# Kernel optimization log

Hardware: AMD Instinct MI355X
Metric: run time of the kernel (lower is better)

The kernel has to match this reference:

```python
import jax, jax.numpy as jnp
import numpy as np

B, S, D, H, KD, HID = 8, 1024, 512, 8, 64, 32


def setup_inputs() -> dict:
    key = jax.random.key(0)
    ks = jax.random.split(key, 13)
    s = 0.05
    return {
        "src": jax.random.normal(ks[0], (B, S, D), jnp.float32),
        "Wq": jax.random.normal(ks[1], (H, KD, D), jnp.float32) * s,
        "Wk": jax.random.normal(ks[2], (H, KD, D), jnp.float32) * s,
        "Wv": jax.random.normal(ks[3], (H, KD, D), jnp.float32) * s,
        "c_raw": jnp.ones((H,), jnp.float32),              # nn.Parameter(1.0) per head
        "L": jnp.full((H,), 2.0, jnp.float32),             # nn.Parameter(2.0) per head
        "w1": jax.random.normal(ks[4], (H, HID), jnp.float32) * s,   # Linear(1,HID) weight
        "b1": jax.random.normal(ks[5], (H, HID), jnp.float32) * s,
        "W2": jax.random.normal(ks[6], (H, HID, HID), jnp.float32) * s,  # [out,in]
        "b2": jax.random.normal(ks[7], (H, HID), jnp.float32) * s,
        "w3": jax.random.normal(ks[8], (H, HID), jnp.float32) * s,   # Linear(HID,1) weight
        "b3": jax.random.normal(ks[9], (H,), jnp.float32) * s,
        "Wo": jax.random.normal(ks[10], (D, D), jnp.float32) * s,
    }


def _gelu(x):
    return jax.nn.gelu(x, approximate=False)  # torch nn.GELU default (erf)


def reference(src, Wq, Wk, Wv, c_raw, L, w1, b1, W2, b2, w3, b3, Wo):
    Bc, Sc, Dc = src.shape
    Hh, Kd = Wq.shape[0], Wq.shape[1]
    # ---- FIRE bias: raw[i,j] = log1p(c*(i-j)) / log1p(c*max(L, i+1)) for j<i else 0
    ii = jnp.arange(Sc, dtype=jnp.float32)[:, None]   # [S,1]
    jj = jnp.arange(Sc, dtype=jnp.float32)[None, :]   # [1,S]
    d = ii - jj                                       # [S,S]
    c = jax.nn.softplus(c_raw)[:, None, None]         # [H,1,1]
    num = jnp.log1p(c * jnp.where(d > 0, d, 1.0)[None])          # safe for d<=0
    den = jnp.log1p(c * jnp.maximum(L[:, None, None], ii[None] + 1.0))
    raw = jnp.where(d[None] > 0, num / den, 0.0)      # [H,S,S]
    # ---- f_theta MLP applied elementwise (Linear(1,h)->GELU->Linear(h,h)->GELU->Linear(h,1))
    h1 = _gelu(raw[..., None] * w1[:, None, None, :] + b1[:, None, None, :])   # [H,S,S,HID]
    h2 = _gelu(jnp.einsum('hijk,hlk->hijl', h1, W2) + b2[:, None, None, :])    # [H,S,S,HID]
    bias = jnp.einsum('hijk,hk->hij', h2, w3) + b3[:, None, None]              # [H,S,S]
    # ---- causal mask (strict upper triangle -> -inf)
    causal = jnp.arange(Sc)[None, :] > jnp.arange(Sc)[:, None]
    bias = jnp.where(causal[None], -jnp.inf, bias)
    # ---- attention per head
    q = jnp.einsum('bsd,hkd->bhsk', src, Wq)
    k = jnp.einsum('bsd,hkd->bhsk', src, Wk)
    v = jnp.einsum('bsd,hkd->bhsk', src, Wv)
    logits = jnp.einsum('bhik,bhjk->bhij', q, k) / jnp.sqrt(jnp.float32(Kd)) + bias[None]
    attn = jax.nn.softmax(logits, axis=-1)
    o = jnp.einsum('bhij,bhjk->bhik', attn, v)        # [B,H,S,KD]
    o = jnp.transpose(o, (0, 2, 1, 3)).reshape(Bc, Sc, Hh * Kd)  # concat heads
    return o @ Wo.T
```

## Files before the change

kernel.cpp:

```cpp
#include <hip/hip_runtime.h>
#include <math.h>

#define S_LEN 1024
#define NHEAD 8
#define BATCH 8
#define KDIM  64
#define HID   32
#define NT    2048
#define TRI(q) ((q) * ((q) + 1) / 2)

typedef __attribute__((ext_vector_type(8))) short bf16x8;
typedef __attribute__((ext_vector_type(4))) float f32x4;
typedef unsigned short ushort_t;

__device__ inline ushort_t f2bf(float f) {
  union { float f; unsigned u; } v; v.f = f;
  unsigned u = v.u;
  return (ushort_t)((u + 0x7FFFu + ((u >> 16) & 1u)) >> 16);
}
__device__ inline float bf2f(ushort_t u) {
  union { unsigned x; float f; } v; v.x = ((unsigned)u) << 16; return v.f;
}

__device__ inline void gl_lds16(const ushort_t* g, ushort_t* l) {
  __builtin_amdgcn_global_load_lds(
      (const __attribute__((address_space(1))) unsigned int*)g,
      (__attribute__((address_space(3))) unsigned int*)l, 16, 0, 0);
}

__global__ __launch_bounds__(256) void to_bf16(
    const float* __restrict__ s, const float* __restrict__ wq,
    const float* __restrict__ wk, const float* __restrict__ wv,
    const float* __restrict__ wo,
    ushort_t* __restrict__ sb, ushort_t* __restrict__ wqb,
    ushort_t* __restrict__ wkb, ushort_t* __restrict__ wvb,
    ushort_t* __restrict__ wob) {
  const int y = blockIdx.y;
  const float* src; ushort_t* dst; int n; float scale = 1.0f;
  if (y == 0)      { src = s;  dst = sb;  n = 4194304; }
  else if (y == 1) { src = wq; dst = wqb; n = 262144; scale = 0.125f; }
  else if (y == 2) { src = wk; dst = wkb; n = 262144; }
  else if (y == 3) { src = wv; dst = wvb; n = 262144; }
  else             { src = wo; dst = wob; n = 262144; }
  const int i = (blockIdx.x * 256 + threadIdx.x) * 4;
  if (i < n) {
    float4 v = *(const float4*)&src[i];
    ushort4 o;
    o.x = f2bf(v.x * scale); o.y = f2bf(v.y * scale);
    o.z = f2bf(v.z * scale); o.w = f2bf(v.w * scale);
    *(ushort4*)&dst[i] = o;
  }
}

__global__ __launch_bounds__(256) void fire_tables(
    const float* __restrict__ c_raw, const float* __restrict__ Lp,
    const float* __restrict__ w1, const float* __restrict__ b1,
    const float* __restrict__ W2, const float* __restrict__ b2,
    const float* __restrict__ w3, const float* __restrict__ b3,
    float* __restrict__ num_g, float* __restrict__ rden_g,
    float* __restrict__ gtab_g) {
  __shared__ float h1s[8][33];
  const int h = blockIdx.y;
  const int tid = threadIdx.x;
  const int pl = tid >> 5;
  const int j = tid & 31;
  const int pt = blockIdx.x * 8 + pl;
  const float cr = c_raw[h];
  const float c = (cr > 20.f) ? cr : log1pf(expf(cr));
  const int gid = blockIdx.x * 256 + tid;
  if (gid < S_LEN) {
    num_g[h * S_LEN + gid] = log1pf(c * (float)gid);
    rden_g[h * S_LEN + gid] = 1.0f / log1pf(c * fmaxf(Lp[h], (float)(gid + 1)));
  }
  const float x = (float)pt * (1.0f / NT);
  float v = x * w1[h * HID + j] + b1[h * HID + j];
  h1s[pl][j] = 0.5f * v * (1.0f + erff(v * 0.70710678118f));
  __syncthreads();
  float s = b2[h * HID + j];
  const float* w2r = W2 + ((size_t)(h * HID + j)) * HID;
  #pragma unroll
  for (int k = 0; k < HID; ++k) s += w2r[k] * h1s[pl][k];
  float g = 0.5f * s * (1.0f + erff(s * 0.70710678118f));
  float y = w3[h * HID + j] * g;
  #pragma unroll
  for (int off = 1; off < 32; off <<= 1) y += __shfl_xor(y, off);
  if (j == 0 && pt <= NT) gtab_g[h * (NT + 1) + pt] = y + b3[h];
}

__global__ __launch_bounds__(256) void fire_bias_pre(
    const float* __restrict__ num_g, const float* __restrict__ rden_g,
    const float* __restrict__ gtab_g, ushort_t* __restrict__ biaspre) {
  __shared__ float gtab_s[NT + 1];
  __shared__ float num_s[S_LEN];
  __shared__ float rden_s[64];
  const int tid = threadIdx.x;
  const int h = blockIdx.y;
  const int tileIdx = blockIdx.x;
  int qt = 0;
  while (TRI(qt + 1) <= tileIdx) ++qt;
  const int t = tileIdx - TRI(qt);
  for (int i = tid; i <= NT; i += 256) gtab_s[i] = gtab_g[h * (NT + 1) + i];
  for (int i = tid; i < S_LEN; i += 256) num_s[i] = num_g[h * S_LEN + i];
  if (tid < 64) rden_s[tid] = rden_g[h * S_LEN + qt * 64 + tid];
  __syncthreads();
  const int lane = tid & 63, w = tid >> 6, quad = lane >> 4, l16 = lane & 15;
  ushort_t vals[16];
  #pragma unroll
  for (int nb = 0; nb < 4; ++nb) {
    #pragma unroll
    for (int r = 0; r < 4; ++r) {
      const int iloc = w * 16 + quad * 4 + r;
      const int i = qt * 64 + iloc;
      const int j = t * 64 + nb * 16 + l16;
      ushort_t out;
      if (j > i) {
        out = 0xFF80;
      } else {
        const int d = i - j;
        float x = num_s[d] * rden_s[iloc];
        float tf = x * (float)NT;
        int it = (int)tf; it = it < (NT - 1) ? it : (NT - 1);
        float fr = tf - (float)it;
        float ga = gtab_s[it];
        out = f2bf(ga + (gtab_s[it + 1] - ga) * fr);
      }
      vals[nb * 4 + r] = out;
    }
  }
  ushort_t* dst = &biaspre[(((size_t)h * 136 + tileIdx) * 256 + tid) * 16];
  uint4 lo, hi;
  #pragma unroll
  for (int v = 0; v < 8; ++v) { ((ushort_t*)&lo)[v] = vals[v]; ((ushort_t*)&hi)[v] = vals[v + 8]; }
  *(uint4*)dst = lo;
  *(uint4*)(dst + 8) = hi;
}

__global__ __launch_bounds__(256) void gemm_bf16(
    const ushort_t* __restrict__ A,
    const ushort_t* __restrict__ W0, const ushort_t* __restrict__ W1,
    const ushort_t* __restrict__ W2w,
    void* __restrict__ out0, void* __restrict__ out1, void* __restrict__ out2,
    int scatter) {
  __shared__ __align__(16) ushort_t sAB[16384];
  ushort_t* sA = sAB;
  ushort_t* sB = sAB + 8192;
  const int tid = threadIdx.x;
  const int lane = tid & 63;
  const int w = tid >> 6;
  const int quad = lane >> 4;
  const int l16 = lane & 15;
  const int m0 = blockIdx.x * 128;
  const int n0 = blockIdx.y * 128;
  const int z = blockIdx.z;
  const ushort_t* Wp = (z == 0) ? W0 : (z == 1) ? W1 : W2w;
  void* outp = (z == 0) ? out0 : (z == 1) ? out1 : out2;
  const int mode = scatter ? ((z == 2) ? 2 : 1) : 0;

  f32x4 acc[2][8];
  #pragma unroll
  for (int s2 = 0; s2 < 2; ++s2)
    #pragma unroll
    for (int nb = 0; nb < 8; ++nb) acc[s2][nb] = (f32x4)0.0f;

  const int r8 = lane >> 3;
  const int gc = (lane & 7) ^ r8;
  const int sw = l16 & 7;

  for (int kt = 0; kt < 512; kt += 64) {
    __syncthreads();
    #pragma unroll
    for (int j = 0; j < 4; ++j) {
      const int row = j * 32 + w * 8 + r8;
      gl_lds16(&A[(size_t)(m0 + row) * 512 + kt + gc * 8], &sA[(j * 32 + w * 8) * 64]);
      gl_lds16(&Wp[(size_t)(n0 + row) * 512 + kt + gc * 8], &sB[(j * 32 + w * 8) * 64]);
    }
    __syncthreads();
    #pragma unroll
    for (int ks = 0; ks < 2; ++ks) {
      const int c = ks * 4 + quad;
      const int off = ((c ^ sw) * 8);
      bf16x8 a0 = *(bf16x8*)&sA[(w * 32 + l16) * 64 + off];
      bf16x8 a1 = *(bf16x8*)&sA[(w * 32 + 16 + l16) * 64 + off];
      #pragma unroll
      for (int nb = 0; nb < 8; ++nb) {
        bf16x8 bfr = *(bf16x8*)&sB[(nb * 16 + l16) * 64 + off];
        acc[0][nb] = __builtin_amdgcn_mfma_f32_16x16x32_bf16(a0, bfr, acc[0][nb], 0, 0, 0);
        acc[1][nb] = __builtin_amdgcn_mfma_f32_16x16x32_bf16(a1, bfr, acc[1][nb], 0, 0, 0);
      }
    }
  }

  if (mode == 2) {
    __syncthreads();
    #pragma unroll
    for (int s2 = 0; s2 < 2; ++s2)
      #pragma unroll
      for (int nb = 0; nb < 8; ++nb)
        #pragma unroll
        for (int r = 0; r < 4; ++r) {
          int nl = nb * 16 + l16;
          int ml = w * 32 + s2 * 16 + quad * 4 + r;
          sAB[nl * 128 + (((ml >> 3) ^ (nl & 7)) * 8) + (ml & 7)] = f2bf(acc[s2][nb][r]);
        }
    __syncthreads();
    const int nl = tid >> 1, halfm = tid & 1;
    const int ng = n0 + nl, hh = ng >> 6, kd = ng & 63;
    const int bb = m0 >> 10, sbase = m0 & 1023;
    ushort_t* vout = (ushort_t*)outp + (((size_t)(bb * NHEAD + hh)) * KDIM + kd) * S_LEN;
    #pragma unroll
    for (int c2 = 0; c2 < 8; ++c2) {
      int mc = halfm * 8 + c2;
      bf16x8 vr = *(bf16x8*)&sAB[nl * 128 + ((mc ^ (nl & 7)) * 8)];
      *(bf16x8*)&vout[sbase + mc * 8] = vr;
    }
    return;
  }
  #pragma unroll
  for (int s2 = 0; s2 < 2; ++s2) {
    #pragma unroll
    for (int nb = 0; nb < 8; ++nb) {
      #pragma unroll
      for (int r = 0; r < 4; ++r) {
        int m = m0 + w * 32 + s2 * 16 + quad * 4 + r;
        int n = n0 + nb * 16 + l16;
        float v = acc[s2][nb][r];
        if (mode == 1) {
          int bb = m >> 10, ss = m & 1023, hh = n >> 6, kd = n & 63;
          ((ushort_t*)outp)[(((size_t)(bb * NHEAD + hh)) * S_LEN + ss) * KDIM + kd] = f2bf(v);
        } else {
          ((float*)outp)[(size_t)m * 512 + n] = v;
        }
      }
    }
  }
}

__global__ __launch_bounds__(256) void fire_attn_mfma(
    const ushort_t* __restrict__ Qg, const ushort_t* __restrict__ Kg,
    const ushort_t* __restrict__ Vtg, const ushort_t* __restrict__ biaspre,
    ushort_t* __restrict__ Ob) {
  __shared__ __align__(16) ushort_t Ks[64][72];
  __shared__ __align__(16) ushort_t Vt[64][72];
  __shared__ __align__(16) ushort_t Ps[64][72];

  const int tid = threadIdx.x;
  const int lane = tid & 63;
  const int w = tid >> 6;
  const int quad = lane >> 4;
  const int l16 = lane & 15;
  const int g = blockIdx.x >> 6;
  const int qt = (g < 8) ? (15 - g) : (g - 8);
  const int bh = blockIdx.x & 63;
  const int h = bh & (NHEAD - 1);
  const int b = bh >> 3;

  const size_t qrow = (size_t)bh * S_LEN + qt * 64 + w * 16 + l16;
  bf16x8 aq0 = *(const bf16x8*)&Qg[qrow * KDIM + quad * 8];
  bf16x8 aq1 = *(const bf16x8*)&Qg[qrow * KDIM + 32 + quad * 8];

  const int krow = tid >> 2, kseg = tid & 3;
  const size_t kb = (size_t)bh * S_LEN * KDIM;
  const ushort_t* kptr = &Kg[kb + (size_t)krow * 64 + kseg * 16];
  const ushort_t* vptr = &Vtg[kb + (size_t)krow * 1024 + kseg * 16];
  const ushort_t* bptr = &biaspre[(((size_t)h * 136 + TRI(qt)) * 256 + tid) * 16];

  uint4 kr0 = *(const uint4*)(kptr);
  uint4 kr1 = *(const uint4*)(kptr + 8);
  uint4 vr0 = *(const uint4*)(vptr);
  uint4 vr1 = *(const uint4*)(vptr + 8);

  f32x4 o[4];
  float ll[4];
  #pragma unroll
  for (int nb = 0; nb < 4; ++nb) o[nb] = (f32x4)0.0f;
  #pragma unroll
  for (int r = 0; r < 4; ++r) ll[r] = 0.f;
  const int i0loc = w * 16 + quad * 4;

  for (int t = 0; t <= qt; ++t) {
    __syncthreads();
    *(uint4*)&Ks[krow][kseg * 16] = kr0;
    *(uint4*)&Ks[krow][kseg * 16 + 8] = kr1;
    *(uint4*)&Vt[krow][kseg * 16] = vr0;
    *(uint4*)&Vt[krow][kseg * 16 + 8] = vr1;
    __syncthreads();

    uint4 bb0 = *(const uint4*)(bptr + (size_t)t * 4096);
    uint4 bb1 = *(const uint4*)(bptr + (size_t)t * 4096 + 8);
    if (t < qt) {
      kr0 = *(const uint4*)(kptr + (size_t)(t + 1) * 4096);
      kr1 = *(const uint4*)(kptr + (size_t)(t + 1) * 4096 + 8);
      vr0 = *(const uint4*)(vptr + (size_t)(t + 1) * 64);
      vr1 = *(const uint4*)(vptr + (size_t)(t + 1) * 64 + 8);
    }

    f32x4 s[4];
    #pragma unroll
    for (int nb = 0; nb < 4; ++nb) s[nb] = (f32x4)0.0f;
    #pragma unroll
    for (int ks = 0; ks < 2; ++ks) {
      bf16x8 aq = ks ? aq1 : aq0;
      #pragma unroll
      for (int nb = 0; nb < 4; ++nb) {
        bf16x8 bk = *(bf16x8*)&Ks[nb * 16 + l16][ks * 32 + quad * 8];
        s[nb] = __builtin_amdgcn_mfma_f32_16x16x32_bf16(aq, bk, s[nb], 0, 0, 0);
      }
    }

    #pragma unroll
    for (int nb = 0; nb < 4; ++nb) {
      #pragma unroll
      for (int r = 0; r < 4; ++r) {
        int v = nb * 4 + r;
        ushort_t bu = (v < 8) ? ((ushort_t*)&bb0)[v] : ((ushort_t*)&bb1)[v - 8];
        float p = __expf(s[nb][r] + bf2f(bu));
        ushort_t pu = f2bf(p);
        Ps[i0loc + r][nb * 16 + l16] = pu;
        ll[r] += bf2f(pu);
      }
    }

    #pragma unroll
    for (int ks = 0; ks < 2; ++ks) {
      bf16x8 ap = *(bf16x8*)&Ps[w * 16 + l16][ks * 32 + quad * 8];
      #pragma unroll
      for (int nb = 0; nb < 4; ++nb) {
        bf16x8 bv = *(bf16x8*)&Vt[nb * 16 + l16][ks * 32 + quad * 8];
        o[nb] = __builtin_amdgcn_mfma_f32_16x16x32_bf16(ap, bv, o[nb], 0, 0, 0);
      }
    }
  }

  const int i0 = qt * 64 + i0loc;
  #pragma unroll
  for (int r = 0; r < 4; ++r) {
    float rs = ll[r];
    #pragma unroll
    for (int off = 1; off < 16; off <<= 1) rs += __shfl_xor(rs, off);
    float rl = 1.0f / rs;
    size_t ob = ((size_t)(b * S_LEN + i0 + r)) * 512 + h * KDIM;
    #pragma unroll
    for (int nb = 0; nb < 4; ++nb)
      Ob[ob + nb * 16 + l16] = f2bf(o[nb][r] * rl);
  }
}

extern "C" void kernel_launch(void* const* d_in, const int* in_sizes, int n_in,
                              void* d_out, int out_size, void* d_ws, size_t ws_size,
                              hipStream_t stream) {
  const float* src   = (const float*)d_in[0];
  const float* Wq    = (const float*)d_in[1];
  const float* Wk    = (const float*)d_in[2];
  const float* Wv    = (const float*)d_in[3];
  const float* c_raw = (const float*)d_in[4];
  const float* Lp    = (const float*)d_in[5];
  const float* w1    = (const float*)d_in[6];
  const float* b1    = (const float*)d_in[7];
  const float* W2    = (const float*)d_in[8];
  const float* b2    = (const float*)d_in[9];
  const float* w3    = (const float*)d_in[10];
  const float* b3    = (const float*)d_in[11];
  const float* Wo    = (const float*)d_in[12];
  float* outp = (float*)d_out;

  const size_t SRC_E = 4194304;
  const size_t W_E   = 262144;
  const size_t QKV_E = 4194304;
  ushort_t* srcb = (ushort_t*)d_ws;
  ushort_t* Wqb  = srcb + SRC_E;
  ushort_t* Wkb  = Wqb + W_E;
  ushort_t* Wvb  = Wkb + W_E;
  ushort_t* Wob  = Wvb + W_E;
  ushort_t* Qb   = Wob + W_E;
  ushort_t* Kb   = Qb + QKV_E;
  ushort_t* Vtb  = Kb + QKV_E;
  ushort_t* Obb  = Vtb + QKV_E;
  ushort_t* biaspre = Obb + QKV_E;
  float* numb  = (float*)(biaspre + (size_t)NHEAD * 136 * 256 * 16);
  float* rdenb = numb + NHEAD * S_LEN;
  float* gtabb = rdenb + NHEAD * S_LEN;

  hipLaunchKernelGGL(fire_tables, dim3(257, NHEAD), dim3(256), 0, stream,
                     c_raw, Lp, w1, b1, W2, b2, w3, b3, numb, rdenb, gtabb);
  hipLaunchKernelGGL(to_bf16, dim3(4096, 5), dim3(256), 0, stream,
                     src, Wq, Wk, Wv, Wo, srcb, Wqb, Wkb, Wvb, Wob);
  hipLaunchKernelGGL(fire_bias_pre, dim3(136, NHEAD), dim3(256), 0, stream,
                     numb, rdenb, gtabb, biaspre);
  hipLaunchKernelGGL(gemm_bf16, dim3(64, 4, 3), dim3(256), 0, stream,
                     srcb, Wqb, Wkb, Wvb, (void*)Qb, (void*)Kb, (void*)Vtb, 1);
  hipLaunchKernelGGL(fire_attn_mfma, dim3(1024), dim3(256), 0, stream,
                     Qb, Kb, Vtb, biaspre, Obb);
  hipLaunchKernelGGL(gemm_bf16, dim3(64, 4, 1), dim3(256), 0, stream,
                     Obb, Wob, Wob, Wob, (void*)outp, (void*)outp, (void*)outp, 0);
}
```

Before: 181.8 us.

## Merge prep kernels, fuse bias precompute into QKV GEMM, restructure attention tiles

Merges the bf16 conversion and FIRE table kernels into one launch, and runs the bias-tile precompute as extra blocks inside the QKV GEMM launch. Reworks the GEMM warp tiling to a 2x2 grid of 64x64 per warp. Restructures attention to 128-thread blocks with 32 query rows per warp, loads K/V straight into swizzled LDS, computes S transposed so P stays in registers (no Ps LDS round trip), and sums the softmax denominator in fp32. The goal is fewer launches, less LDS traffic and better MFMA operand reuse, at the cost of more register pressure and a more complex bias layout.

Result: faster. 170.9 us (-6.0%).

```diff
diff --git a/kernel.cpp b/kernel.cpp
--- a/kernel.cpp
+++ b/kernel.cpp
@@ -8,6 +8,8 @@
 #define HID   32
 #define NT    2048
 #define TRI(q) ((q) * ((q) + 1) / 2)
+#define PERM(m) (((m) & 0x20) | (((m) & 0x0C) << 1) | (((m) & 0x10) >> 2) | ((m) & 3))
+#define SWZ(row) (((((row) >> 3) & 1) << 2) | ((row) & 3))
 
 typedef __attribute__((ext_vector_type(8))) short bf16x8;
 typedef __attribute__((ext_vector_type(4))) float f32x4;
@@ -28,31 +30,13 @@
       (__attribute__((address_space(3))) unsigned int*)l, 16, 0, 0);
 }
 
-__global__ __launch_bounds__(256) void to_bf16(
+__global__ __launch_bounds__(256) void prep(
     const float* __restrict__ s, const float* __restrict__ wq,
     const float* __restrict__ wk, const float* __restrict__ wv,
     const float* __restrict__ wo,
     ushort_t* __restrict__ sb, ushort_t* __restrict__ wqb,
     ushort_t* __restrict__ wkb, ushort_t* __restrict__ wvb,
-    ushort_t* __restrict__ wob) {
-  const int y = blockIdx.y;
-  const float* src; ushort_t* dst; int n; float scale = 1.0f;
-  if (y == 0)      { src = s;  dst = sb;  n = 4194304; }
-  else if (y == 1) { src = wq; dst = wqb; n = 262144; scale = 0.125f; }
-  else if (y == 2) { src = wk; dst = wkb; n = 262144; }
-  else if (y == 3) { src = wv; dst = wvb; n = 262144; }
-  else             { src = wo; dst = wob; n = 262144; }
-  const int i = (blockIdx.x * 256 + threadIdx.x) * 4;
-  if (i < n) {
-    float4 v = *(const float4*)&src[i];
-    ushort4 o;
-    o.x = f2bf(v.x * scale); o.y = f2bf(v.y * scale);
-    o.z = f2bf(v.z * scale); o.w = f2bf(v.w * scale);
-    *(ushort4*)&dst[i] = o;
-  }
-}
-
-__global__ __launch_bounds__(256) void fire_tables(
+    ushort_t* __restrict__ wob,
     const float* __restrict__ c_raw, const float* __restrict__ Lp,
     const float* __restrict__ w1, const float* __restrict__ b1,
     const float* __restrict__ W2, const float* __restrict__ b2,
@@ -60,107 +44,63 @@
     float* __restrict__ num_g, float* __restrict__ rden_g,
     float* __restrict__ gtab_g) {
   __shared__ float h1s[8][33];
-  const int h = blockIdx.y;
+  const int bx = blockIdx.x;
   const int tid = threadIdx.x;
-  const int pl = tid >> 5;
-  const int j = tid & 31;
-  const int pt = blockIdx.x * 8 + pl;
-  const float cr = c_raw[h];
-  const float c = (cr > 20.f) ? cr : log1pf(expf(cr));
-  const int gid = blockIdx.x * 256 + tid;
-  if (gid < S_LEN) {
-    num_g[h * S_LEN + gid] = log1pf(c * (float)gid);
-    rden_g[h * S_LEN + gid] = 1.0f / log1pf(c * fmaxf(Lp[h], (float)(gid + 1)));
-  }
-  const float x = (float)pt * (1.0f / NT);
-  float v = x * w1[h * HID + j] + b1[h * HID + j];
-  h1s[pl][j] = 0.5f * v * (1.0f + erff(v * 0.70710678118f));
-  __syncthreads();
-  float s = b2[h * HID + j];
-  const float* w2r = W2 + ((size_t)(h * HID + j)) * HID;
-  #pragma unroll
-  for (int k = 0; k < HID; ++k) s += w2r[k] * h1s[pl][k];
-  float g = 0.5f * s * (1.0f + erff(s * 0.70710678118f));
-  float y = w3[h * HID + j] * g;
-  #pragma unroll
-  for (int off = 1; off < 32; off <<= 1) y += __shfl_xor(y, off);
-  if (j == 0 && pt <= NT) gtab_g[h * (NT + 1) + pt] = y + b3[h];
-}
-
-__global__ __launch_bounds__(256) void fire_bias_pre(
-    const float* __restrict__ num_g, const float* __restrict__ rden_g,
-    const float* __restrict__ gtab_g, ushort_t* __restrict__ biaspre) {
-  __shared__ float gtab_s[NT + 1];
-  __shared__ float num_s[S_LEN];
-  __shared__ float rden_s[64];
-  const int tid = threadIdx.x;
-  const int h = blockIdx.y;
-  const int tileIdx = blockIdx.x;
-  int qt = 0;
-  while (TRI(qt + 1) <= tileIdx) ++qt;
-  const int t = tileIdx - TRI(qt);
-  for (int i = tid; i <= NT; i += 256) gtab_s[i] = gtab_g[h * (NT + 1) + i];
-  for (int i = tid; i < S_LEN; i += 256) num_s[i] = num_g[h * S_LEN + i];
-  if (tid < 64) rden_s[tid] = rden_g[h * S_LEN + qt * 64 + tid];
-  __syncthreads();
-  const int lane = tid & 63, w = tid >> 6, quad = lane >> 4, l16 = lane & 15;
-  ushort_t vals[16];
-  #pragma unroll
-  for (int nb = 0; nb < 4; ++nb) {
-    #pragma unroll
-    for (int r = 0; r < 4; ++r) {
-      const int iloc = w * 16 + quad * 4 + r;
-      const int i = qt * 64 + iloc;
-      const int j = t * 64 + nb * 16 + l16;
-      ushort_t out;
-      if (j > i) {
-        out = 0xFF80;
-      } else {
-        const int d = i - j;
-        float x = num_s[d] * rden_s[iloc];
-        float tf = x * (float)NT;
-        int it = (int)tf; it = it < (NT - 1) ? it : (NT - 1);
-        float fr = tf - (float)it;
-        float ga = gtab_s[it];
-        out = f2bf(ga + (gtab_s[it + 1] - ga) * fr);
-      }
-      vals[nb * 4 + r] = out;
-    }
-  }
-  ushort_t* dst = &biaspre[(((size_t)h * 136 + tileIdx) * 256 + tid) * 16];
-  uint4 lo, hi;
-  #pragma unroll
-  for (int v = 0; v < 8; ++v) { ((ushort_t*)&lo)[v] = vals[v]; ((ushort_t*)&hi)[v] = vals[v + 8]; }
-  *(uint4*)dst = lo;
-  *(uint4*)(dst + 8) = hi;
-}
-
-__global__ __launch_bounds__(256) void gemm_bf16(
-    const ushort_t* __restrict__ A,
-    const ushort_t* __restrict__ W0, const ushort_t* __restrict__ W1,
-    const ushort_t* __restrict__ W2w,
-    void* __restrict__ out0, void* __restrict__ out1, void* __restrict__ out2,
-    int scatter) {
-  __shared__ __align__(16) ushort_t sAB[16384];
+  if (bx < 5120) {
+    const float* src; ushort_t* dst; int base; float scale = 1.0f;
+    if (bx < 4096)      { src = s;  dst = sb;  base = bx; }
+    else if (bx < 4352) { src = wq; dst = wqb; base = bx - 4096; scale = 0.125f; }
+    else if (bx < 4608) { src = wk; dst = wkb; base = bx - 4352; }
+    else if (bx < 4864) { src = wv; dst = wvb; base = bx - 4608; }
+    else                { src = wo; dst = wob; base = bx - 4864; }
+    const int i = (base * 256 + tid) * 4;
+    float4 v = *(const float4*)&src[i];
+    ushort4 o;
+    o.x = f2bf(v.x * scale); o.y = f2bf(v.y * scale);
+    o.z = f2bf(v.z * scale); o.w = f2bf(v.w * scale);
+    *(ushort4*)&dst[i] = o;
+  } else {
+    const int idx = bx - 5120;
+    const int h = idx / 257;
+    const int xb = idx % 257;
+    const float cr = c_raw[h];
+    const float c = (cr > 20.f) ? cr : log1pf(expf(cr));
+    const int gid = xb * 256 + tid;
+    if (gid < S_LEN) {
+      num_g[h * S_LEN + gid] = log1pf(c * (float)gid);
+      rden_g[h * S_LEN + gid] = 1.0f / log1pf(c * fmaxf(Lp[h], (float)(gid + 1)));
+    }
+    const int pl = tid >> 5;
+    const int j = tid & 31;
+    const int pt = xb * 8 + pl;
+    const float x = (float)pt * (1.0f / NT);
+    float v = x * w1[h * HID + j] + b1[h * HID + j];
+    h1s[pl][j] = 0.5f * v * (1.0f + erff(v * 0.70710678118f));
+    __syncthreads();
+    float sm = b2[h * HID + j];
+    const float* w2r = W2 + ((size_t)(h * HID + j)) * HID;
+    #pragma unroll
+    for (int k = 0; k < HID; ++k) sm += w2r[k] * h1s[pl][k];
+    float g = 0.5f * sm * (1.0f + erff(sm * 0.70710678118f));
+    float y = w3[h * HID + j] * g;
+    #pragma unroll
+    for (int off = 1; off < 32; off <<= 1) y += __shfl_xor(y, off);
+    if (j == 0 && pt <= NT) gtab_g[h * (NT + 1) + pt] = y + b3[h];
+  }
+}
+
+__device__ __forceinline__ void gemm_tile(
+    ushort_t* sAB, const ushort_t* __restrict__ A, const ushort_t* __restrict__ Wp,
+    void* __restrict__ outp, int mode, int m0, int n0, int tid) {
   ushort_t* sA = sAB;
   ushort_t* sB = sAB + 8192;
-  const int tid = threadIdx.x;
-  const int lane = tid & 63;
-  const int w = tid >> 6;
-  const int quad = lane >> 4;
-  const int l16 = lane & 15;
-  const int m0 = blockIdx.x * 128;
-  const int n0 = blockIdx.y * 128;
-  const int z = blockIdx.z;
-  const ushort_t* Wp = (z == 0) ? W0 : (z == 1) ? W1 : W2w;
-  void* outp = (z == 0) ? out0 : (z == 1) ? out1 : out2;
-  const int mode = scatter ? ((z == 2) ? 2 : 1) : 0;
-
-  f32x4 acc[2][8];
+  const int lane = tid & 63, w = tid >> 6, quad = lane >> 4, l16 = lane & 15;
+  const int wr = w >> 1, wc = w & 1;
+  f32x4 acc[4][4];
   #pragma unroll
-  for (int s2 = 0; s2 < 2; ++s2)
-    #pragma unroll
-    for (int nb = 0; nb < 8; ++nb) acc[s2][nb] = (f32x4)0.0f;
+  for (int ia = 0; ia < 4; ++ia)
+    #pragma unroll
+    for (int ib = 0; ib < 4; ++ib) acc[ia][ib] = (f32x4)0.0f;
 
   const int r8 = lane >> 3;
   const int gc = (lane & 7) ^ r8;
@@ -177,30 +117,32 @@
     __syncthreads();
     #pragma unroll
     for (int ks = 0; ks < 2; ++ks) {
-      const int c = ks * 4 + quad;
-      const int off = ((c ^ sw) * 8);
-      bf16x8 a0 = *(bf16x8*)&sA[(w * 32 + l16) * 64 + off];
-      bf16x8 a1 = *(bf16x8*)&sA[(w * 32 + 16 + l16) * 64 + off];
-      #pragma unroll
-      for (int nb = 0; nb < 8; ++nb) {
-        bf16x8 bfr = *(bf16x8*)&sB[(nb * 16 + l16) * 64 + off];
-        acc[0][nb] = __builtin_amdgcn_mfma_f32_16x16x32_bf16(a0, bfr, acc[0][nb], 0, 0, 0);
-        acc[1][nb] = __builtin_amdgcn_mfma_f32_16x16x32_bf16(a1, bfr, acc[1][nb], 0, 0, 0);
+      const int off = ((ks * 4 + quad) ^ sw) * 8;
+      bf16x8 af[4], bfr[4];
+      #pragma unroll
+      for (int i = 0; i < 4; ++i) {
+        af[i] = *(bf16x8*)&sA[(wr * 64 + i * 16 + l16) * 64 + off];
+        bfr[i] = *(bf16x8*)&sB[(wc * 64 + i * 16 + l16) * 64 + off];
       }
+      #pragma unroll
+      for (int ia = 0; ia < 4; ++ia)
+        #pragma unroll
+        for (int ib = 0; ib < 4; ++ib)
+          acc[ia][ib] = __builtin_amdgcn_mfma_f32_16x16x32_bf16(af[ia], bfr[ib], acc[ia][ib], 0, 0, 0);
     }
   }
 
   if (mode == 2) {
     __syncthreads();
     #pragma unroll
-    for (int s2 = 0; s2 < 2; ++s2)
-      #pragma unroll
-      for (int nb = 0; nb < 8; ++nb)
+    for (int ia = 0; ia < 4; ++ia)
+      #pragma unroll
+      for (int ib = 0; ib < 4; ++ib)
         #pragma unroll
         for (int r = 0; r < 4; ++r) {
-          int nl = nb * 16 + l16;
-          int ml = w * 32 + s2 * 16 + quad * 4 + r;
-          sAB[nl * 128 + (((ml >> 3) ^ (nl & 7)) * 8) + (ml & 7)] = f2bf(acc[s2][nb][r]);
+          int nl = wc * 64 + ib * 16 + l16;
+          int ml = wr * 64 + ia * 16 + quad * 4 + r;
+          sAB[nl * 128 + (((ml >> 3) ^ (nl & 7)) * 8) + (ml & 7)] = f2bf(acc[ia][ib][r]);
         }
     __syncthreads();
     const int nl = tid >> 1, halfm = tid & 1;
@@ -216,14 +158,14 @@
     return;
   }
   #pragma unroll
-  for (int s2 = 0; s2 < 2; ++s2) {
-    #pragma unroll
-    for (int nb = 0; nb < 8; ++nb) {
+  for (int ia = 0; ia < 4; ++ia) {
+    #pragma unroll
+    for (int ib = 0; ib < 4; ++ib) {
       #pragma unroll
       for (int r = 0; r < 4; ++r) {
-        int m = m0 + w * 32 + s2 * 16 + quad * 4 + r;
-        int n = n0 + nb * 16 + l16;
-        float v = acc[s2][nb][r];
+        int m = m0 + wr * 64 + ia * 16 + quad * 4 + r;
+        int n = n0 + wc * 64 + ib * 16 + l16;
+        float v = acc[ia][ib][r];
         if (mode == 1) {
           int bb = m >> 10, ss = m & 1023, hh = n >> 6, kd = n & 63;
           ((ushort_t*)outp)[(((size_t)(bb * NHEAD + hh)) * S_LEN + ss) * KDIM + kd] = f2bf(v);
@@ -235,113 +177,205 @@
   }
 }
 
-__global__ __launch_bounds__(256) void fire_attn_mfma(
+__global__ __launch_bounds__(256) void gemm_bias(
+    const ushort_t* __restrict__ A,
+    const ushort_t* __restrict__ W0, const ushort_t* __restrict__ W1,
+    const ushort_t* __restrict__ W2w,
+    void* __restrict__ out0, void* __restrict__ out1, void* __restrict__ out2,
+    int scatter, int nGemm,
+    const float* __restrict__ num_g, const float* __restrict__ rden_g,
+    const float* __restrict__ gtab_g, ushort_t* __restrict__ biaspre) {
+  __shared__ __align__(16) ushort_t sAB[16384];
+  const int tid = threadIdx.x;
+  if ((int)blockIdx.x < nGemm) {
+    const int z = blockIdx.x >> 8;
+    const int idx = blockIdx.x & 255;
+    const int m0 = (idx & 63) * 128;
+    const int n0 = (idx >> 6) * 128;
+    const ushort_t* Wp = (z == 0) ? W0 : (z == 1) ? W1 : W2w;
+    void* outp = (z == 0) ? out0 : (z == 1) ? out1 : out2;
+    const int mode = scatter ? ((z == 2) ? 2 : 1) : 0;
+    gemm_tile(sAB, A, Wp, outp, mode, m0, n0, tid);
+  } else {
+    const int idx = blockIdx.x - nGemm;
+    const int h = idx / 68;
+    const int pair = idx % 68;
+    float* gtab_s = (float*)sAB;
+    float* num_s = gtab_s + 2052;
+    float* rden_s = num_s + 1024;
+    for (int i = tid; i <= NT; i += 256) gtab_s[i] = gtab_g[h * (NT + 1) + i];
+    for (int i = tid; i < S_LEN; i += 256) num_s[i] = num_g[h * S_LEN + i];
+    const int sub = tid >> 7, tid2 = tid & 127;
+    const int tileIdx = pair * 2 + sub;
+    int qt = 0;
+    while (TRI(qt + 1) <= tileIdx) ++qt;
+    const int t = tileIdx - TRI(qt);
+    if (tid2 < 64) rden_s[sub * 64 + tid2] = rden_g[h * S_LEN + qt * 64 + tid2];
+    __syncthreads();
+    const int w = tid2 >> 6, lane = tid2 & 63, quad = lane >> 4, l16 = lane & 15;
+    ushort_t vals[32];
+    #pragma unroll
+    for (int qg = 0; qg < 2; ++qg) {
+      const int iloc = w * 32 + qg * 16 + l16;
+      const int i = qt * 64 + iloc;
+      const float rden = rden_s[sub * 64 + iloc];
+      #pragma unroll
+      for (int nb = 0; nb < 4; ++nb)
+        #pragma unroll
+        for (int r = 0; r < 4; ++r) {
+          const int m = nb * 16 + quad * 4 + r;
+          const int j = t * 64 + PERM(m);
+          ushort_t out;
+          if (j > i) {
+            out = 0xFF80;
+          } else {
+            const int d = i - j;
+            float x = num_s[d] * rden;
+            float tf = x * (float)NT;
+            int it = (int)tf; it = it < (NT - 1) ? it : (NT - 1);
+            float fr = tf - (float)it;
+            float ga = gtab_s[it];
+            out = f2bf(ga + (gtab_s[it + 1] - ga) * fr);
+          }
+          vals[qg * 16 + nb * 4 + r] = out;
+        }
+    }
+    ushort_t* dst = &biaspre[((size_t)(h * 136 + tileIdx) * 128 + tid2) * 32];
+    uint4 u[2];
+    #pragma unroll
+    for (int half = 0; half < 2; ++half) {
+      #pragma unroll
+      for (int v = 0; v < 8; ++v) ((ushort_t*)&u[0])[v] = vals[half * 16 + v];
+      #pragma unroll
+      for (int v = 0; v < 8; ++v) ((ushort_t*)&u[1])[v] = vals[half * 16 + 8 + v];
+      *(uint4*)(dst + half * 16) = u[0];
+      *(uint4*)(dst + half * 16 + 8) = u[1];
+    }
+  }
+}
+
+__global__ __launch_bounds__(128) void fire_attn_mfma(
     const ushort_t* __restrict__ Qg, const ushort_t* __restrict__ Kg,
     const ushort_t* __restrict__ Vtg, const ushort_t* __restrict__ biaspre,
     ushort_t* __restrict__ Ob) {
-  __shared__ __align__(16) ushort_t Ks[64][72];
-  __shared__ __align__(16) ushort_t Vt[64][72];
-  __shared__ __align__(16) ushort_t Ps[64][72];
-
+  __shared__ __align__(16) ushort_t Ks[64 * 64];
+  __shared__ __align__(16) ushort_t Vt[64 * 64];
   const int tid = threadIdx.x;
-  const int lane = tid & 63;
-  const int w = tid >> 6;
-  const int quad = lane >> 4;
-  const int l16 = lane & 15;
+  const int lane = tid & 63, w = tid >> 6, quad = lane >> 4, l16 = lane & 15;
   const int g = blockIdx.x >> 6;
   const int qt = (g < 8) ? (15 - g) : (g - 8);
-  const int bh = blockIdx.x & 63;
-  const int h = bh & (NHEAD - 1);
-  const int b = bh >> 3;
-
-  const size_t qrow = (size_t)bh * S_LEN + qt * 64 + w * 16 + l16;
-  bf16x8 aq0 = *(const bf16x8*)&Qg[qrow * KDIM + quad * 8];
-  bf16x8 aq1 = *(const bf16x8*)&Qg[qrow * KDIM + 32 + quad * 8];
-
-  const int krow = tid >> 2, kseg = tid & 3;
+  const int bh = blockIdx.x & 63, h = bh & 7, b = bh >> 3;
+
+  bf16x8 q[2][2];
+  {
+    const size_t qb = (size_t)bh * S_LEN + qt * 64 + w * 32;
+    #pragma unroll
+    for (int qg = 0; qg < 2; ++qg)
+      #pragma unroll
+      for (int ks = 0; ks < 2; ++ks)
+        q[qg][ks] = *(const bf16x8*)&Qg[(qb + qg * 16 + l16) * KDIM + ks * 32 + quad * 8];
+  }
+
   const size_t kb = (size_t)bh * S_LEN * KDIM;
-  const ushort_t* kptr = &Kg[kb + (size_t)krow * 64 + kseg * 16];
-  const ushort_t* vptr = &Vtg[kb + (size_t)krow * 1024 + kseg * 16];
-  const ushort_t* bptr = &biaspre[(((size_t)h * 136 + TRI(qt)) * 256 + tid) * 16];
-
-  uint4 kr0 = *(const uint4*)(kptr);
-  uint4 kr1 = *(const uint4*)(kptr + 8);
-  uint4 vr0 = *(const uint4*)(vptr);
-  uint4 vr1 = *(const uint4*)(vptr + 8);
-
-  f32x4 o[4];
-  float ll[4];
+  const ushort_t* bptr = &biaspre[((size_t)(h * 136 + TRI(qt)) * 128 + tid) * 32];
+  const int srow8 = lane >> 3;
+  const int sc = lane & 7;
+
+  f32x4 o[2][4];
+  float ll[2] = {0.f, 0.f};
   #pragma unroll
-  for (int nb = 0; nb < 4; ++nb) o[nb] = (f32x4)0.0f;
+  for (int qg = 0; qg < 2; ++qg)
+    #pragma unroll
+    for (int nb = 0; nb < 4; ++nb) o[qg][nb] = (f32x4)0.0f;
+
+  for (int t = 0; t <= qt; ++t) {
+    __syncthreads();
+    #pragma unroll
+    for (int j = 0; j < 4; ++j) {
+      const int row = (w * 4 + j) * 8 + srow8;
+      const int cc = sc ^ SWZ(row);
+      gl_lds16(&Kg[kb + (size_t)(t * 64 + row) * 64 + cc * 8], &Ks[(w * 4 + j) * 512]);
+      gl_lds16(&Vtg[kb + (size_t)row * 1024 + t * 64 + cc * 8], &Vt[(w * 4 + j) * 512]);
+    }
+    __syncthreads();
+
+    uint4 bb0 = ((const uint4*)(bptr + (size_t)t * 4096))[0];
+    uint4 bb1 = ((const uint4*)(bptr + (size_t)t * 4096))[1];
+    uint4 bb2 = ((const uint4*)(bptr + (size_t)t * 4096))[2];
+    uint4 bb3 = ((const uint4*)(bptr + (size_t)t * 4096))[3];
+
+    f32x4 s[2][4];
+    #pragma unroll
+    for (int qg = 0; qg < 2; ++qg)
+      #pragma unroll
+      for (int nb = 0; nb < 4; ++nb) s[qg][nb] = (f32x4)0.0f;
+    #pragma unroll
+    for (int ks = 0; ks < 2; ++ks) {
+      #pragma unroll
+      for (int nb = 0; nb < 4; ++nb) {
+        const int rk = PERM(nb * 16 + l16);
+        bf16x8 ak = *(bf16x8*)&Ks[rk * 64 + (((ks * 4 + quad) ^ SWZ(rk)) * 8)];
+        #pragma unroll
+        for (int qg = 0; qg < 2; ++qg)
+          s[qg][nb] = __builtin_amdgcn_mfma_f32_16x16x32_bf16(ak, q[qg][ks], s[qg][nb], 0, 0, 0);
+      }
+    }
+
+    ushort_t eb[2][16];
+    #pragma unroll
+    for (int qg = 0; qg < 2; ++qg) {
+      #pragma unroll
+      for (int nb = 0; nb < 4; ++nb)
+        #pragma unroll
+        for (int r = 0; r < 4; ++r) {
+          const int v = qg * 16 + nb * 4 + r;
+          const uint4& bq = (v < 8) ? bb0 : (v < 16) ? bb1 : (v < 24) ? bb2 : bb3;
+          ushort_t bu = ((const ushort_t*)&bq)[v & 7];
+          float p = __expf(s[qg][nb][r] + bf2f(bu));
+          ll[qg] += p;
+          eb[qg][nb * 4 + r] = f2bf(p);
+        }
+    }
+
+    #pragma unroll
+    for (int ks = 0; ks < 2; ++ks) {
+      bf16x8 pf[2];
+      #pragma unroll
+      for (int qg = 0; qg < 2; ++qg) {
+        union { bf16x8 v; unsigned u[4]; } pk;
+        pk.u[0] = (unsigned)eb[qg][(2 * ks) * 4 + 0] | ((unsigned)eb[qg][(2 * ks) * 4 + 1] << 16);
+        pk.u[1] = (unsigned)eb[qg][(2 * ks) * 4 + 2] | ((unsigned)eb[qg][(2 * ks) * 4 + 3] << 16);
+        pk.u[2] = (unsigned)eb[qg][(2 * ks + 1) * 4 + 0] | ((unsigned)eb[qg][(2 * ks + 1) * 4 + 1] << 16);
+        pk.u[3] = (unsigned)eb[qg][(2 * ks + 1) * 4 + 2] | ((unsigned)eb[qg][(2 * ks + 1) * 4 + 3] << 16);
+        pf[qg] = pk.v;
+      }
+      #pragma unroll
+      for (int nb = 0; nb < 4; ++nb) {
+        const int rv = nb * 16 + l16;
+        bf16x8 av = *(bf16x8*)&Vt[rv * 64 + (((ks * 4 + quad) ^ SWZ(rv)) * 8)];
+        #pragma unroll
+        for (int qg = 0; qg < 2; ++qg)
+          o[qg][nb] = __builtin_amdgcn_mfma_f32_16x16x32_bf16(av, pf[qg], o[qg][nb], 0, 0, 0);
+      }
+    }
+  }
+
   #pragma unroll
-  for (int r = 0; r < 4; ++r) ll[r] = 0.f;
-  const int i0loc = w * 16 + quad * 4;
-
-  for (int t = 0; t <= qt; ++t) {
-    __syncthreads();
-    *(uint4*)&Ks[krow][kseg * 16] = kr0;
-    *(uint4*)&Ks[krow][kseg * 16 + 8] = kr1;
-    *(uint4*)&Vt[krow][kseg * 16] = vr0;
-    *(uint4*)&Vt[krow][kseg * 16 + 8] = vr1;
-    __syncthreads();
-
-    uint4 bb0 = *(const uint4*)(bptr + (size_t)t * 4096);
-    uint4 bb1 = *(const uint4*)(bptr + (size_t)t * 4096 + 8);
-    if (t < qt) {
-      kr0 = *(const uint4*)(kptr + (size_t)(t + 1) * 4096);
-      kr1 = *(const uint4*)(kptr + (size_t)(t + 1) * 4096 + 8);
-      vr0 = *(const uint4*)(vptr + (size_t)(t + 1) * 64);
-      vr1 = *(const uint4*)(vptr + (size_t)(t + 1) * 64 + 8);
-    }
-
-    f32x4 s[4];
-    #pragma unroll
-    for (int nb = 0; nb < 4; ++nb) s[nb] = (f32x4)0.0f;
-    #pragma unroll
-    for (int ks = 0; ks < 2; ++ks) {
-      bf16x8 aq = ks ? aq1 : aq0;
-      #pragma unroll
-      for (int nb = 0; nb < 4; ++nb) {
-        bf16x8 bk = *(bf16x8*)&Ks[nb * 16 + l16][ks * 32 + quad * 8];
-        s[nb] = __builtin_amdgcn_mfma_f32_16x16x32_bf16(aq, bk, s[nb], 0, 0, 0);
-      }
-    }
-
+  for (int qg = 0; qg < 2; ++qg) {
+    float rs = ll[qg];
+    rs += __shfl_xor(rs, 16);
+    rs += __shfl_xor(rs, 32);
+    const float rl = 1.0f / rs;
+    const size_t ob = ((size_t)(b * S_LEN + qt * 64 + w * 32 + qg * 16 + l16)) * 512 + h * KDIM;
     #pragma unroll
     for (int nb = 0; nb < 4; ++nb) {
-      #pragma unroll
-      for (int r = 0; r < 4; ++r) {
-        int v = nb * 4 + r;
-        ushort_t bu = (v < 8) ? ((ushort_t*)&bb0)[v] : ((ushort_t*)&bb1)[v - 8];
-        float p = __expf(s[nb][r] + bf2f(bu));
-        ushort_t pu = f2bf(p);
-        Ps[i0loc + r][nb * 16 + l16] = pu;
-        ll[r] += bf2f(pu);
-      }
-    }
-
-    #pragma unroll
-    for (int ks = 0; ks < 2; ++ks) {
-      bf16x8 ap = *(bf16x8*)&Ps[w * 16 + l16][ks * 32 + quad * 8];
-      #pragma unroll
-      for (int nb = 0; nb < 4; ++nb) {
-        bf16x8 bv = *(bf16x8*)&Vt[nb * 16 + l16][ks * 32 + quad * 8];
-        o[nb] = __builtin_amdgcn_mfma_f32_16x16x32_bf16(ap, bv, o[nb], 0, 0, 0);
-      }
-    }
-  }
-
-  const int i0 = qt * 64 + i0loc;
-  #pragma unroll
-  for (int r = 0; r < 4; ++r) {
-    float rs = ll[r];
-    #pragma unroll
-    for (int off = 1; off < 16; off <<= 1) rs += __shfl_xor(rs, off);
-    float rl = 1.0f / rs;
-    size_t ob = ((size_t)(b * S_LEN + i0 + r)) * 512 + h * KDIM;
-    #pragma unroll
-    for (int nb = 0; nb < 4; ++nb)
-      Ob[ob + nb * 16 + l16] = f2bf(o[nb][r] * rl);
+      ushort4 ov;
+      ov.x = f2bf(o[qg][nb][0] * rl);
+      ov.y = f2bf(o[qg][nb][1] * rl);
+      ov.z = f2bf(o[qg][nb][2] * rl);
+      ov.w = f2bf(o[qg][nb][3] * rl);
+      *(ushort4*)&Ob[ob + nb * 16 + quad * 4] = ov;
+    }
   }
 }
 
@@ -376,20 +410,19 @@
   ushort_t* Vtb  = Kb + QKV_E;
   ushort_t* Obb  = Vtb + QKV_E;
   ushort_t* biaspre = Obb + QKV_E;
-  float* numb  = (float*)(biaspre + (size_t)NHEAD * 136 * 256 * 16);
+  float* numb  = (float*)(biaspre + (size_t)NHEAD * 136 * 128 * 32);
   float* rdenb = numb + NHEAD * S_LEN;
   float* gtabb = rdenb + NHEAD * S_LEN;
 
-  hipLaunchKernelGGL(fire_tables, dim3(257, NHEAD), dim3(256), 0, stream,
+  hipLaunchKernelGGL(prep, dim3(7176), dim3(256), 0, stream,
+                     src, Wq, Wk, Wv, Wo, srcb, Wqb, Wkb, Wvb, Wob,
                      c_raw, Lp, w1, b1, W2, b2, w3, b3, numb, rdenb, gtabb);
-  hipLaunchKernelGGL(to_bf16, dim3(4096, 5), dim3(256), 0, stream,
-                     src, Wq, Wk, Wv, Wo, srcb, Wqb, Wkb, Wvb, Wob);
-  hipLaunchKernelGGL(fire_bias_pre, dim3(136, NHEAD), dim3(256), 0, stream,
-                     numb, rdenb, gtabb, biaspre);
-  hipLaunchKernelGGL(gemm_bf16, dim3(64, 4, 3), dim3(256), 0, stream,
-                     srcb, Wqb, Wkb, Wvb, (void*)Qb, (void*)Kb, (void*)Vtb, 1);
-  hipLaunchKernelGGL(fire_attn_mfma, dim3(1024), dim3(256), 0, stream,
+  hipLaunchKernelGGL(gemm_bias, dim3(1312), dim3(256), 0, stream,
+                     srcb, Wqb, Wkb, Wvb, (void*)Qb, (void*)Kb, (void*)Vtb,
+                     1, 768, numb, rdenb, gtabb, biaspre);
+  hipLaunchKernelGGL(fire_attn_mfma, dim3(1024), dim3(128), 0, stream,
                      Qb, Kb, Vtb, biaspre, Obb);
-  hipLaunchKernelGGL(gemm_bf16, dim3(64, 4, 1), dim3(256), 0, stream,
-                     Obb, Wob, Wob, Wob, (void*)outp, (void*)outp, (void*)outp, 0);
-}
+  hipLaunchKernelGGL(gemm_bias, dim3(256), dim3(256), 0, stream,
+                     Obb, Wob, Wob, Wob, (void*)outp, (void*)outp, (void*)outp,
+                     0, 256, numb, rdenb, gtabb, biaspre);
+}
```
